# Kernel tuning notes

Measured on AMD Instinct MI355X. Metric: run time of the kernel, lower is better.

## Reference

```python
import jax, jax.numpy as jnp
import numpy as np

LN_EPS = 1e-12


def setup_inputs() -> dict:
    key = jax.random.key(0)
    ks = jax.random.split(key, 5)
    B, N, D_IN, D_OUT, E = 32, 2048, 128, 128, 64
    return {
        "x": jax.random.normal(ks[0], (B, N, D_IN), dtype=jnp.float32),
        "node_embeddings": jax.random.normal(ks[1], (N, E), dtype=jnp.float32),
        "time_embeddings": jax.random.normal(ks[2], (E,), dtype=jnp.float32),
        "weights_pool": jax.random.normal(ks[3], (E, 2, D_IN, D_OUT), dtype=jnp.float32) * 0.02,
        "bias_pool": jax.random.normal(ks[4], (E, D_OUT), dtype=jnp.float32) * 0.02,
        "ln_weight": jnp.ones((E,), dtype=jnp.float32),
        "ln_bias": jnp.zeros((E,), dtype=jnp.float32),
    }


def reference(x, node_embeddings, time_embeddings, weights_pool, bias_pool, ln_weight, ln_bias):
    # e: [N, E] = LayerNorm(node_emb + time_emb)  (dropout in eval mode = identity)
    e = node_embeddings + time_embeddings[None, :]
    mu = jnp.mean(e, axis=-1, keepdims=True)
    var = jnp.mean(jnp.square(e - mu), axis=-1, keepdims=True)
    e = (e - mu) * jax.lax.rsqrt(var + LN_EPS) * ln_weight + ln_bias

    # adaptive adjacency: softmax over rows of e @ e.T  -> [N, N]
    adj = jax.nn.softmax(jnp.einsum('nd,md->nm', e, e), axis=1)

    # per-node weights [N, 2, I, O] and bias [N, O]
    weights = jnp.einsum('nd,dkio->nkio', e, weights_pool)
    bias = e @ bias_pool  # [N, O]

    # supports: k=0 identity (x itself), k=1 adjacency aggregation
    x_agg = jnp.einsum('nm,bmc->bnc', adj, x)        # [B, N, I]
    x_g = jnp.stack([x, x_agg], axis=2)              # [B, N, 2, I]

    # per-node batched GEMM + bias
    out = jnp.einsum('bnki,nkio->bno', x_g, weights) + bias
    return out
```

## Files before the change

kernel.cpp:

```cpp
#include <hip/hip_runtime.h>


typedef unsigned short u16;
typedef unsigned int u32;
typedef __attribute__((ext_vector_type(8))) short bf16x8;
typedef __attribute__((ext_vector_type(4))) float f32x4;
typedef const __attribute__((address_space(1))) u16* gas1;
typedef __attribute__((address_space(3))) u16* las3;

#define NN 2048
#define EE 64
#define CC 128
#define BB 32

__device__ __forceinline__ u16 f2bf(float f) {
  u32 u = __builtin_bit_cast(u32, f);
  u += 0x7fffu + ((u >> 16) & 1u);
  return (u16)(u >> 16);
}

__device__ __forceinline__ f32x4 mfma16(bf16x8 a, bf16x8 b, f32x4 c) {
  return __builtin_amdgcn_mfma_f32_16x16x32_bf16(a, b, c, 0, 0, 0);
}

__global__ __launch_bounds__(256) void k_mega0(
    const float* __restrict__ x, const float* __restrict__ ne,
    const float* __restrict__ te, const float* __restrict__ pool,
    const float* __restrict__ bias_pool, const float* __restrict__ lnw,
    const float* __restrict__ lnb,
    float* __restrict__ e, u16* __restrict__ e_bf, float* __restrict__ bias_out,
    u16* __restrict__ pool_r, u16* __restrict__ x_t, u16* __restrict__ xg_t) {
  __shared__ __align__(16) char smem[34048];
  int bid = blockIdx.x;
  int tid = threadIdx.x;
  if (bid < 512) {
    float* sh = (float*)smem;
    int nw = tid >> 6, d = tid & 63;
    int n = bid * 4 + nw;
    float v = ne[n * EE + d] + te[d];
    float s = v;
#pragma unroll
    for (int off = 32; off > 0; off >>= 1) s += __shfl_xor(s, off);
    float mean = s * (1.0f / 64.0f);
    float c = v - mean;
    float q = c * c;
#pragma unroll
    for (int off = 32; off > 0; off >>= 1) q += __shfl_xor(q, off);
    float inv = rsqrtf(q * (1.0f / 64.0f) + 1e-12f);
    float ev = c * inv * lnw[d] + lnb[d];
    e[n * EE + d] = ev;
    e_bf[n * EE + d] = f2bf(ev);
    sh[nw * 64 + d] = ev;
    __syncthreads();
#pragma unroll
    for (int oo = 0; oo < 2; ++oo) {
      int o = oo * 64 + d;
      float acc = 0.f;
#pragma unroll 8
      for (int dd = 0; dd < 64; ++dd) acc += sh[nw * 64 + dd] * bias_pool[dd * CC + o];
      bias_out[n * CC + o] = acc;
    }
  } else if (bid < 768) {
    float* t = (float*)smem;
    int ki = bid - 512;
    for (int it = 0; it < 32; ++it) {
      int idx = it * 256 + tid;
      int d = idx >> 7, o = idx & 127;
      t[o * 65 + d] = pool[d * 32768 + ki * 128 + o];
    }
    __syncthreads();
    for (int it = 0; it < 32; ++it) {
      int idx = it * 256 + tid;
      int o = idx >> 6, d = idx & 63;
      pool_r[((size_t)o * 256 + ki) * 64 + d] = f2bf(t[o * 65 + d]);
    }
  } else {
    u16* t = (u16*)smem;
    int bx = bid - 768;
    int b = bx >> 5;
    int m0 = (bx & 31) * 64;
    for (int it = 0; it < 32; ++it) {
      int idx = it * 256 + tid;
      int m = idx >> 7, c = idx & 127;
      float v = x[((size_t)b * NN + m0 + m) * CC + c];
      t[c * 68 + m] = f2bf(v);
    }
    __syncthreads();
    for (int it = 0; it < 32; ++it) {
      int idx = it * 256 + tid;
      int c = idx >> 6, m = idx & 63;
      x_t[((size_t)b * CC + c) * NN + m0 + m] = t[c * 68 + m];
    }
    for (int it = 0; it < 16; ++it) {
      int idx = it * 256 + tid;
      int m = idx >> 6, c2 = idx & 63;
      float2 v = *(const float2*)&x[((size_t)b * NN + m0 + m) * CC + c2 * 2];
      u32 pk = (u32)f2bf(v.x) | ((u32)f2bf(v.y) << 16);
      *(u32*)&xg_t[(((size_t)(m0 + m)) * 32 + b) * 256 + c2 * 2] = pk;
    }
  }
}

__global__ __launch_bounds__(256) void k_Sexp(const float* __restrict__ e,
                                              u16* __restrict__ P,
                                              float* __restrict__ rs) {
  __shared__ float er[64 * 68];
  __shared__ float ec[64 * 68];
  int n0 = (blockIdx.x >> 5) * 64, m0 = (blockIdx.x & 31) * 64;
  int tid = threadIdx.x;
  for (int it = 0; it < 16; ++it) {
    int idx = it * 256 + tid;
    int r = idx >> 6, d = idx & 63;
    er[r * 68 + d] = e[(n0 + r) * EE + d];
    ec[r * 68 + d] = e[(m0 + r) * EE + d];
  }
  __syncthreads();
  int tx = tid & 15, ty = tid >> 4;
  float acc[4][4] = {};
  for (int d4 = 0; d4 < 64; d4 += 4) {
    f32x4 av[4], bv[4];
#pragma unroll
    for (int i = 0; i < 4; ++i) av[i] = *(const f32x4*)&er[(ty + 16 * i) * 68 + d4];
#pragma unroll
    for (int j = 0; j < 4; ++j) bv[j] = *(const f32x4*)&ec[(tx + 16 * j) * 68 + d4];
#pragma unroll
    for (int i = 0; i < 4; ++i)
#pragma unroll
      for (int j = 0; j < 4; ++j) {
        acc[i][j] += av[i][0] * bv[j][0];
        acc[i][j] += av[i][1] * bv[j][1];
        acc[i][j] += av[i][2] * bv[j][2];
        acc[i][j] += av[i][3] * bv[j][3];
      }
  }
#pragma unroll
  for (int i = 0; i < 4; ++i) {
    float s = 0.f;
#pragma unroll
    for (int j = 0; j < 4; ++j) {
      float pv = __expf(acc[i][j]);
      P[(size_t)(n0 + ty + 16 * i) * NN + m0 + tx + 16 * j] = f2bf(pv);
      s += pv;
    }
#pragma unroll
    for (int off = 8; off > 0; off >>= 1) s += __shfl_xor(s, off);
    if (tx == 0) atomicAdd(&rs[n0 + ty + 16 * i], s);
  }
}

__global__ __launch_bounds__(256, 4) void k_mega2(
    const u16* __restrict__ P, const u16* __restrict__ x_t,
    const float* __restrict__ rs, u16* __restrict__ xg_t,
    const u16* __restrict__ e_bf, const u16* __restrict__ pool_r,
    u16* __restrict__ W_p) {
  __shared__ __align__(16) char smem[34048];
  int tid = threadIdx.x;
  int lane = tid & 63, w = tid >> 6;
  int lm = lane & 15, lq = lane >> 4;
  if (blockIdx.x < 512) {
    u16* As = (u16*)smem;
    u16* Bs = (u16*)(smem + 16384);
    int mb = blockIdx.x & 15, b = blockIdx.x >> 4;
    int n0 = mb * 128;
    int wm = w >> 1, wn = w & 1;
    f32x4 acc[4][4] = {};
    const u16* a_src = P + (size_t)n0 * NN;
    const u16* b_src = x_t + (size_t)b * CC * NN;
    for (int kc = 0; kc < NN; kc += 64) {
      __syncthreads();
#pragma unroll
      for (int ii = 0; ii < 4; ++ii) {
        int idx = ii * 256 + tid;
        int row = idx >> 3, ch = idx & 7;
        int sc = kc + ((ch ^ (row & 7)) << 3);
        __builtin_amdgcn_global_load_lds((gas1)(a_src + (size_t)row * NN + sc),
                                         (las3)(As + (size_t)(ii * 256 + w * 64) * 8), 16, 0, 0);
        __builtin_amdgcn_global_load_lds((gas1)(b_src + (size_t)row * NN + sc),
                                         (las3)(Bs + (size_t)(ii * 256 + w * 64) * 8), 16, 0, 0);
      }
      __syncthreads();
#pragma unroll
      for (int kk = 0; kk < 64; kk += 32) {
        int cb = (kk >> 3) + lq;
        bf16x8 af[4], bq[4];
#pragma unroll
        for (int i = 0; i < 4; ++i) {
          int row = wm * 64 + i * 16 + lm;
          af[i] = *(const bf16x8*)&As[row * 64 + ((cb ^ (row & 7)) << 3)];
        }
#pragma unroll
        for (int j = 0; j < 4; ++j) {
          int row = wn * 64 + j * 16 + lm;
          bq[j] = *(const bf16x8*)&Bs[row * 64 + ((cb ^ (row & 7)) << 3)];
        }
#pragma unroll
        for (int i = 0; i < 4; ++i)
#pragma unroll
          for (int j = 0; j < 4; ++j)
            acc[i][j] = mfma16(af[i], bq[j], acc[i][j]);
      }
    }
#pragma unroll
    for (int i = 0; i < 4; ++i) {
      int nr = n0 + wm * 64 + i * 16 + lq * 4;
#pragma unroll
      for (int r = 0; r < 4; ++r) {
        float sc = 1.0f / rs[nr + r];
#pragma unroll
        for (int j = 0; j < 4; ++j) {
          int c = wn * 64 + j * 16 + lm;
          xg_t[((size_t)(nr + r) * 32 + b) * 256 + 128 + c] = f2bf(acc[i][j][r] * sc);
        }
      }
    }
  } else {
    u16* Tl = (u16*)smem;
    int g = blockIdx.x - 512;
    int og = g & 63, nb = g >> 6;
    int o0 = og * 2, n0 = nb * 32;
    int o_l = w & 1, kih = w >> 1;
    bf16x8 eB[2][2];
#pragma unroll
    for (int nt = 0; nt < 2; ++nt)
#pragma unroll
      for (int ks = 0; ks < 2; ++ks)
        eB[nt][ks] = *(const bf16x8*)&e_bf[(n0 + nt * 16 + lm) * EE + ks * 32 + lq * 8];
    const u16* pbase = pool_r + ((size_t)(o0 + o_l) * 256 + kih * 128) * 64;
#pragma unroll
    for (int ct = 0; ct < 8; ++ct) {
      const u16* ap = pbase + (ct * 16 + lm) * 64 + lq * 8;
      bf16x8 pA0 = *(const bf16x8*)ap;
      bf16x8 pA1 = *(const bf16x8*)(ap + 32);
#pragma unroll
      for (int nt = 0; nt < 2; ++nt) {
        f32x4 gv = {0.f, 0.f, 0.f, 0.f};
        gv = mfma16(pA0, eB[nt][0], gv);
        gv = mfma16(pA1, eB[nt][1], gv);
        ushort4 h;
        h.x = f2bf(gv[0]); h.y = f2bf(gv[1]); h.z = f2bf(gv[2]); h.w = f2bf(gv[3]);
        *(ushort4*)&Tl[o_l * 8456 + (nt * 16 + lm) * 264 + kih * 128 + ct * 16 + lq * 4] = h;
      }
    }
    __syncthreads();
#pragma unroll
    for (int it = 0; it < 8; ++it) {
      int idx = it * 256 + tid;
      int n = idx >> 6, rem = idx & 63;
      int ks = rem >> 3, rem2 = rem & 7;
      int o = rem2 >> 2, ki8 = rem2 & 3;
      uint4 v = *(const uint4*)&Tl[o * 8456 + n * 264 + ks * 32 + ki8 * 8];
      *(uint4*)&W_p[(size_t)(n0 + n) * 32768 + ks * 4096 + (o0 + o) * 32 + ki8 * 8] = v;
    }
  }
}

__global__ __launch_bounds__(256, 3) void k_apply(const u16* __restrict__ xg_t,
                                                  const u16* __restrict__ W_p,
                                                  const float* __restrict__ bias,
                                                  float* __restrict__ out) {
  __shared__ float L[2 * 32 * 132];
  int n0 = blockIdx.x * 2;
  int tid = threadIdx.x;
  int lane = tid & 63, w = tid >> 6;
  int lm = lane & 15, lq = lane >> 4;
  int n = n0 + (w & 1), oh = w >> 1;
  const u16* xb = xg_t + (size_t)n * 32 * 256;
  const u16* wb = W_p + (size_t)n * 32768 + (size_t)oh * 64 * 32;
  f32x4 acc[2][4] = {};
#pragma unroll
  for (int ks = 0; ks < 8; ++ks) {
    int ko = ks * 32 + lq * 8;
    bf16x8 a0 = *(const bf16x8*)&xb[lm * 256 + ko];
    bf16x8 a1 = *(const bf16x8*)&xb[(16 + lm) * 256 + ko];
#pragma unroll
    for (int ot = 0; ot < 4; ++ot) {
      bf16x8 bv = *(const bf16x8*)&wb[(size_t)ks * 4096 + (ot * 16 + lm) * 32 + lq * 8];
      acc[0][ot] = mfma16(a0, bv, acc[0][ot]);
      acc[1][ot] = mfma16(a1, bv, acc[1][ot]);
    }
  }
#pragma unroll
  for (int ot = 0; ot < 4; ++ot) {
    int oc = oh * 64 + ot * 16 + lm;
#pragma unroll
    for (int mt = 0; mt < 2; ++mt)
#pragma unroll
      for (int r = 0; r < 4; ++r) {
        int b = mt * 16 + lq * 4 + r;
        L[((w & 1) * 32 + b) * 132 + oc] = acc[mt][ot][r];
      }
  }
  __syncthreads();
#pragma unroll
  for (int it = 0; it < 8; ++it) {
    int idx = it * 256 + tid;
    int row = idx >> 5, seg = idx & 31;
    int nl = row >> 5, b = row & 31;
    float4 v = *(const float4*)&L[(nl * 32 + b) * 132 + seg * 4];
    float4 bv = *(const float4*)&bias[(n0 + nl) * CC + seg * 4];
    float4 o4;
    o4.x = v.x + bv.x; o4.y = v.y + bv.y; o4.z = v.z + bv.z; o4.w = v.w + bv.w;
    *(float4*)&out[((size_t)b * NN + n0 + nl) * CC + seg * 4] = o4;
  }
}

extern "C" void kernel_launch(void* const* d_in, const int* in_sizes, int n_in,
                              void* d_out, int out_size, void* d_ws, size_t ws_size,
                              hipStream_t stream) {
  const float* x        = (const float*)d_in[0];
  const float* node_emb = (const float*)d_in[1];
  const float* time_emb = (const float*)d_in[2];
  const float* pool     = (const float*)d_in[3];
  const float* bias_pl  = (const float*)d_in[4];
  const float* ln_w     = (const float*)d_in[5];
  const float* ln_b     = (const float*)d_in[6];
  float* out = (float*)d_out;

  char* p = (char*)d_ws;
  auto alloc = [&](size_t bytes) {
    char* r = p;
    p += (bytes + 255) & ~(size_t)255;
    return r;
  };
  float* e      = (float*)alloc((size_t)NN * EE * 4);
  u16*   e_bf   = (u16*)  alloc((size_t)NN * EE * 2);
  float* biasb  = (float*)alloc((size_t)NN * CC * 4);
  u16*   Pm     = (u16*)  alloc((size_t)NN * NN * 2);
  float* rs     = (float*)alloc((size_t)NN * 4);
  u16*   x_t    = (u16*)  alloc((size_t)BB * CC * NN * 2);
  u16*   xg_t   = (u16*)  alloc((size_t)NN * BB * 256 * 2);
  u16*   pool_r = (u16*)  alloc((size_t)128 * 256 * 64 * 2);
  u16*   W_p    = (u16*)  alloc((size_t)NN * 32768 * 2);

  if (ws_size < (size_t)(p - (char*)d_ws)) return;

  (void)hipMemsetAsync(rs, 0, (size_t)NN * 4, stream);

  k_mega0<<<1792, 256, 0, stream>>>(x, node_emb, time_emb, pool, bias_pl, ln_w, ln_b,
                                    e, e_bf, biasb, pool_r, x_t, xg_t);
  k_Sexp<<<1024, 256, 0, stream>>>(e, Pm, rs);
  k_mega2<<<4608, 256, 0, stream>>>(Pm, x_t, rs, xg_t, e_bf, pool_r, W_p);
  k_apply<<<NN / 2, 256, 0, stream>>>(xg_t, W_p, biasb, out);
}
```

Baseline: 231.2 us.

## Fuse LayerNorm+exp-score kernel into prep megakernel and double-buffer aggregation GEMM

The separate k_Sexp launch is removed. Its score/exp blocks move into k_mega0 and recompute the LayerNorm of their row and column tiles, so the fp32 e buffer and one kernel launch go away. The aggregation GEMM in k_mega2 now double-buffers its LDS tiles: the next k-chunk is loaded while MFMAs run on the current one. That doubles shared memory to 64KB and lowers the launch-bounds occupancy hint from 4 to 2 blocks, which may reduce latency hiding for the other k_mega2 branch.

New measurement: 269.9 us. +16.7%, slower.

```diff
diff --git a/kernel.cpp b/kernel.cpp
--- a/kernel.cpp
+++ b/kernel.cpp
@@ -28,15 +28,110 @@
     const float* __restrict__ te, const float* __restrict__ pool,
     const float* __restrict__ bias_pool, const float* __restrict__ lnw,
     const float* __restrict__ lnb,
-    float* __restrict__ e, u16* __restrict__ e_bf, float* __restrict__ bias_out,
-    u16* __restrict__ pool_r, u16* __restrict__ x_t, u16* __restrict__ xg_t) {
-  __shared__ __align__(16) char smem[34048];
+    u16* __restrict__ e_bf, float* __restrict__ bias_out,
+    u16* __restrict__ pool_r, u16* __restrict__ x_t, u16* __restrict__ xg_t,
+    u16* __restrict__ P, float* __restrict__ rs) {
+  __shared__ __align__(16) char smem[34816];
   int bid = blockIdx.x;
   int tid = threadIdx.x;
-  if (bid < 512) {
+  if (bid < 1024) {
+    float* er = (float*)smem;
+    float* ec = (float*)(smem + 17408);
+    int n0 = (bid >> 5) * 64, m0 = (bid & 31) * 64;
+    int nw = tid >> 6, d = tid & 63;
+    float tev = te[d], lw = lnw[d], lb = lnb[d];
+#pragma unroll 4
+    for (int p = 0; p < 32; ++p) {
+      int ri = p * 4 + nw;
+      int n = ri < 64 ? n0 + ri : m0 + (ri - 64);
+      float v = ne[n * EE + d] + tev;
+      float s = v;
+#pragma unroll
+      for (int off = 32; off > 0; off >>= 1) s += __shfl_xor(s, off);
+      float mean = s * (1.0f / 64.0f);
+      float c = v - mean;
+      float q = c * c;
+#pragma unroll
+      for (int off = 32; off > 0; off >>= 1) q += __shfl_xor(q, off);
+      float inv = rsqrtf(q * (1.0f / 64.0f) + 1e-12f);
+      float ev = c * inv * lw + lb;
+      if (ri < 64) er[ri * 68 + d] = ev;
+      else         ec[(ri - 64) * 68 + d] = ev;
+    }
+    __syncthreads();
+    int tx = tid & 15, ty = tid >> 4;
+    float acc[4][4] = {};
+    for (int d4 = 0; d4 < 64; d4 += 4) {
+      f32x4 av[4], bv[4];
+#pragma unroll
+      for (int i = 0; i < 4; ++i) av[i] = *(const f32x4*)&er[(ty + 16 * i) * 68 + d4];
+#pragma unroll
+      for (int j = 0; j < 4; ++j) bv[j] = *(const f32x4*)&ec[(tx + 16 * j) * 68 + d4];
+#pragma unroll
+      for (int i = 0; i < 4; ++i)
+#pragma unroll
+        for (int j = 0; j < 4; ++j) {
+          acc[i][j] += av[i][0] * bv[j][0];
+          acc[i][j] += av[i][1] * bv[j][1];
+          acc[i][j] += av[i][2] * bv[j][2];
+          acc[i][j] += av[i][3] * bv[j][3];
+        }
+    }
+#pragma unroll
+    for (int i = 0; i < 4; ++i) {
+      float s = 0.f;
+#pragma unroll
+      for (int j = 0; j < 4; ++j) {
+        float pv = __expf(acc[i][j]);
+        P[(size_t)(n0 + ty + 16 * i) * NN + m0 + tx + 16 * j] = f2bf(pv);
+        s += pv;
+      }
+#pragma unroll
+      for (int off = 8; off > 0; off >>= 1) s += __shfl_xor(s, off);
+      if (tx == 0) atomicAdd(&rs[n0 + ty + 16 * i], s);
+    }
+  } else if (bid < 2048) {
+    u16* t = (u16*)smem;
+    int bx = bid - 1024;
+    int b = bx >> 5;
+    int m0 = (bx & 31) * 64;
+    for (int it = 0; it < 32; ++it) {
+      int idx = it * 256 + tid;
+      int m = idx >> 7, c = idx & 127;
+      float v = x[((size_t)b * NN + m0 + m) * CC + c];
+      t[c * 68 + m] = f2bf(v);
+    }
+    __syncthreads();
+    for (int it = 0; it < 32; ++it) {
+      int idx = it * 256 + tid;
+      int c = idx >> 6, m = idx & 63;
+      x_t[((size_t)b * CC + c) * NN + m0 + m] = t[c * 68 + m];
+    }
+    for (int it = 0; it < 16; ++it) {
+      int idx = it * 256 + tid;
+      int m = idx >> 6, c2 = idx & 63;
+      float2 v = *(const float2*)&x[((size_t)b * NN + m0 + m) * CC + c2 * 2];
+      u32 pk = (u32)f2bf(v.x) | ((u32)f2bf(v.y) << 16);
+      *(u32*)&xg_t[(((size_t)(m0 + m)) * 32 + b) * 256 + c2 * 2] = pk;
+    }
+  } else if (bid < 2304) {
+    float* t = (float*)smem;
+    int ki = bid - 2048;
+    for (int it = 0; it < 32; ++it) {
+      int idx = it * 256 + tid;
+      int d = idx >> 7, o = idx & 127;
+      t[o * 65 + d] = pool[d * 32768 + ki * 128 + o];
+    }
+    __syncthreads();
+    for (int it = 0; it < 32; ++it) {
+      int idx = it * 256 + tid;
+      int o = idx >> 6, d = idx & 63;
+      pool_r[((size_t)o * 256 + ki) * 64 + d] = f2bf(t[o * 65 + d]);
+    }
+  } else {
     float* sh = (float*)smem;
     int nw = tid >> 6, d = tid & 63;
-    int n = bid * 4 + nw;
+    int n = (bid - 2304) * 4 + nw;
     float v = ne[n * EE + d] + te[d];
     float s = v;
 #pragma unroll
@@ -48,7 +143,6 @@
     for (int off = 32; off > 0; off >>= 1) q += __shfl_xor(q, off);
     float inv = rsqrtf(q * (1.0f / 64.0f) + 1e-12f);
     float ev = c * inv * lnw[d] + lnb[d];
-    e[n * EE + d] = ev;
     e_bf[n * EE + d] = f2bf(ev);
     sh[nw * 64 + d] = ev;
     __syncthreads();
@@ -60,114 +154,28 @@
       for (int dd = 0; dd < 64; ++dd) acc += sh[nw * 64 + dd] * bias_pool[dd * CC + o];
       bias_out[n * CC + o] = acc;
     }
-  } else if (bid < 768) {
-    float* t = (float*)smem;
-    int ki = bid - 512;
-    for (int it = 0; it < 32; ++it) {
-      int idx = it * 256 + tid;
-      int d = idx >> 7, o = idx & 127;
-      t[o * 65 + d] = pool[d * 32768 + ki * 128 + o];
-    }
-    __syncthreads();
-    for (int it = 0; it < 32; ++it) {
-      int idx = it * 256 + tid;
-      int o = idx >> 6, d = idx & 63;
-      pool_r[((size_t)o * 256 + ki) * 64 + d] = f2bf(t[o * 65 + d]);
-    }
-  } else {
-    u16* t = (u16*)smem;
-    int bx = bid - 768;
-    int b = bx >> 5;
-    int m0 = (bx & 31) * 64;
-    for (int it = 0; it < 32; ++it) {
-      int idx = it * 256 + tid;
-      int m = idx >> 7, c = idx & 127;
-      float v = x[((size_t)b * NN + m0 + m) * CC + c];
-      t[c * 68 + m] = f2bf(v);
-    }
-    __syncthreads();
-    for (int it = 0; it < 32; ++it) {
-      int idx = it * 256 + tid;
-      int c = idx >> 6, m = idx & 63;
-      x_t[((size_t)b * CC + c) * NN + m0 + m] = t[c * 68 + m];
-    }
-    for (int it = 0; it < 16; ++it) {
-      int idx = it * 256 + tid;
-      int m = idx >> 6, c2 = idx & 63;
-      float2 v = *(const float2*)&x[((size_t)b * NN + m0 + m) * CC + c2 * 2];
-      u32 pk = (u32)f2bf(v.x) | ((u32)f2bf(v.y) << 16);
-      *(u32*)&xg_t[(((size_t)(m0 + m)) * 32 + b) * 256 + c2 * 2] = pk;
-    }
-  }
-}
-
-__global__ __launch_bounds__(256) void k_Sexp(const float* __restrict__ e,
-                                              u16* __restrict__ P,
-                                              float* __restrict__ rs) {
-  __shared__ float er[64 * 68];
-  __shared__ float ec[64 * 68];
-  int n0 = (blockIdx.x >> 5) * 64, m0 = (blockIdx.x & 31) * 64;
-  int tid = threadIdx.x;
-  for (int it = 0; it < 16; ++it) {
-    int idx = it * 256 + tid;
-    int r = idx >> 6, d = idx & 63;
-    er[r * 68 + d] = e[(n0 + r) * EE + d];
-    ec[r * 68 + d] = e[(m0 + r) * EE + d];
-  }
-  __syncthreads();
-  int tx = tid & 15, ty = tid >> 4;
-  float acc[4][4] = {};
-  for (int d4 = 0; d4 < 64; d4 += 4) {
-    f32x4 av[4], bv[4];
-#pragma unroll
-    for (int i = 0; i < 4; ++i) av[i] = *(const f32x4*)&er[(ty + 16 * i) * 68 + d4];
-#pragma unroll
-    for (int j = 0; j < 4; ++j) bv[j] = *(const f32x4*)&ec[(tx + 16 * j) * 68 + d4];
-#pragma unroll
-    for (int i = 0; i < 4; ++i)
-#pragma unroll
-      for (int j = 0; j < 4; ++j) {
-        acc[i][j] += av[i][0] * bv[j][0];
-        acc[i][j] += av[i][1] * bv[j][1];
-        acc[i][j] += av[i][2] * bv[j][2];
-        acc[i][j] += av[i][3] * bv[j][3];
-      }
-  }
-#pragma unroll
-  for (int i = 0; i < 4; ++i) {
-    float s = 0.f;
-#pragma unroll
-    for (int j = 0; j < 4; ++j) {
-      float pv = __expf(acc[i][j]);
-      P[(size_t)(n0 + ty + 16 * i) * NN + m0 + tx + 16 * j] = f2bf(pv);
-      s += pv;
-    }
-#pragma unroll
-    for (int off = 8; off > 0; off >>= 1) s += __shfl_xor(s, off);
-    if (tx == 0) atomicAdd(&rs[n0 + ty + 16 * i], s);
-  }
-}
-
-__global__ __launch_bounds__(256, 4) void k_mega2(
+  }
+}
+
+__global__ __launch_bounds__(256, 2) void k_mega2(
     const u16* __restrict__ P, const u16* __restrict__ x_t,
     const float* __restrict__ rs, u16* __restrict__ xg_t,
     const u16* __restrict__ e_bf, const u16* __restrict__ pool_r,
     u16* __restrict__ W_p) {
-  __shared__ __align__(16) char smem[34048];
+  __shared__ __align__(16) char smem[65536];
   int tid = threadIdx.x;
   int lane = tid & 63, w = tid >> 6;
   int lm = lane & 15, lq = lane >> 4;
   if (blockIdx.x < 512) {
-    u16* As = (u16*)smem;
-    u16* Bs = (u16*)(smem + 16384);
     int mb = blockIdx.x & 15, b = blockIdx.x >> 4;
     int n0 = mb * 128;
     int wm = w >> 1, wn = w & 1;
     f32x4 acc[4][4] = {};
     const u16* a_src = P + (size_t)n0 * NN;
     const u16* b_src = x_t + (size_t)b * CC * NN;
-    for (int kc = 0; kc < NN; kc += 64) {
-      __syncthreads();
+    auto STAGE = [&](int kc, char* buf) {
+      u16* As = (u16*)buf;
+      u16* Bs = (u16*)(buf + 16384);
 #pragma unroll
       for (int ii = 0; ii < 4; ++ii) {
         int idx = ii * 256 + tid;
@@ -178,7 +186,14 @@
         __builtin_amdgcn_global_load_lds((gas1)(b_src + (size_t)row * NN + sc),
                                          (las3)(Bs + (size_t)(ii * 256 + w * 64) * 8), 16, 0, 0);
       }
-      __syncthreads();
+    };
+    STAGE(0, smem);
+    __syncthreads();
+    for (int t = 0; t < 32; ++t) {
+      if (t < 31) STAGE((t + 1) * 64, smem + (((t + 1) & 1) << 15));
+      char* cur = smem + ((t & 1) << 15);
+      u16* As = (u16*)cur;
+      u16* Bs = (u16*)(cur + 16384);
 #pragma unroll
       for (int kk = 0; kk < 64; kk += 32) {
         int cb = (kk >> 3) + lq;
@@ -199,6 +214,7 @@
           for (int j = 0; j < 4; ++j)
             acc[i][j] = mfma16(af[i], bq[j], acc[i][j]);
       }
+      __syncthreads();
     }
 #pragma unroll
     for (int i = 0; i < 4; ++i) {
@@ -322,7 +338,6 @@
     p += (bytes + 255) & ~(size_t)255;
     return r;
   };
-  float* e      = (float*)alloc((size_t)NN * EE * 4);
   u16*   e_bf   = (u16*)  alloc((size_t)NN * EE * 2);
   float* biasb  = (float*)alloc((size_t)NN * CC * 4);
   u16*   Pm     = (u16*)  alloc((size_t)NN * NN * 2);
@@ -336,9 +351,8 @@
 
   (void)hipMemsetAsync(rs, 0, (size_t)NN * 4, stream);
 
-  k_mega0<<<1792, 256, 0, stream>>>(x, node_emb, time_emb, pool, bias_pl, ln_w, ln_b,
-                                    e, e_bf, biasb, pool_r, x_t, xg_t);
-  k_Sexp<<<1024, 256, 0, stream>>>(e, Pm, rs);
+  k_mega0<<<2816, 256, 0, stream>>>(x, node_emb, time_emb, pool, bias_pl, ln_w, ln_b,
+                                    e_bf, biasb, pool_r, x_t, xg_t, Pm, rs);
   k_mega2<<<4608, 256, 0, stream>>>(Pm, x_t, rs, xg_t, e_bf, pool_r, W_p);
   k_apply<<<NN / 2, 256, 0, stream>>>(xg_t, W_p, biasb, out);
 }
```
